# Kernel optimization log

Measured on AMD Instinct MI355X. Metric: run time of the kernel, lower is better.

## Reference

```python
import jax, jax.numpy as jnp
import numpy as np

B, S, D, H = 2, 2048, 512, 8
HD = D // H
DFF = 4 * D
EPS_LN = 1e-5
EPS_ATTN = 1e-8


def layernorm(x, w, b):
    mu = jnp.mean(x, axis=-1, keepdims=True)
    var = jnp.var(x, axis=-1, keepdims=True)
    return (x - mu) * jax.lax.rsqrt(var + EPS_LN) * w + b


def masked_attention(q_src, v_src, wq, bq, wk, bk, wv, bv, wo, bo, M):
    # q_src/v_src: (B,S,D); M: (B,S,S)
    Bs, Ss, _ = q_src.shape
    Q = (q_src @ wq + bq).reshape(Bs, Ss, H, HD)
    K = (q_src @ wk + bk).reshape(Bs, Ss, H, HD)
    V = (v_src @ wv + bv).reshape(Bs, Ss, H, HD)
    scale = HD ** -0.5
    scores = jnp.einsum('bqhd,bkhd->bhqk', Q, K) * scale
    Mh = M[:, None, :, :]                      # (B,1,S,S) broadcast over heads
    scores = scores * Mh
    A = jax.nn.softmax(scores, axis=-1)
    A = A * Mh                                 # re-mask post-softmax
    A = A / (jnp.sum(jnp.abs(A), axis=-1, keepdims=True) + EPS_ATTN)  # L1 renorm
    out = jnp.einsum('bhqk,bkhd->bqhd', A, V).reshape(Bs, Ss, D)
    return out @ wo + bo


def ffn(x, w1, b1, w2, b2):
    h = jax.nn.gelu(x @ w1 + b1, approximate=False)
    return x + (h @ w2 + b2)                   # FeedForward(num_layers=2) includes residual


def setup_inputs() -> dict:
    key = jax.random.key(0)
    ks = iter(jax.random.split(key, 64))
    nrm = lambda shape, s=0.02: jax.random.normal(next(ks), shape, jnp.float32) * s
    d = {
        'gene_emb': jax.random.normal(next(ks), (B, S, D), jnp.float32),
        'expr_emb': jax.random.normal(next(ks), (B, S, D), jnp.float32),
        'M': jax.random.uniform(next(ks), (B, S, S), jnp.float32),
    }
    # gene attention params (weights stored (in,out))
    for p in ['g_wq', 'g_wk', 'g_wv', 'g_wo']:
        d[p] = nrm((D, D))
    for p in ['g_bq', 'g_bk', 'g_bv', 'g_bo']:
        d[p] = jnp.zeros((D,), jnp.float32)
    # expr attention params (fused proj 2D->D)
    d['e_wf'] = nrm((2 * D, D)); d['e_bf'] = jnp.zeros((D,), jnp.float32)
    for p in ['e_wq', 'e_wk', 'e_wv', 'e_wo']:
        d[p] = nrm((D, D))
    for p in ['e_bq', 'e_bk', 'e_bv', 'e_bo']:
        d[p] = jnp.zeros((D,), jnp.float32)
    # layernorms
    for p in ['ln_g1_w', 'ln_g2_w', 'ln_e1_w', 'ln_e2_w']:
        d[p] = jnp.ones((D,), jnp.float32)
    for p in ['ln_g1_b', 'ln_g2_b', 'ln_e1_b', 'ln_e2_b']:
        d[p] = jnp.zeros((D,), jnp.float32)
    # FFNs
    d['fg_w1'] = nrm((D, DFF)); d['fg_b1'] = jnp.zeros((DFF,), jnp.float32)
    d['fg_w2'] = nrm((DFF, D)); d['fg_b2'] = jnp.zeros((D,), jnp.float32)
    d['fe_w1'] = nrm((D, DFF)); d['fe_b1'] = jnp.zeros((DFF,), jnp.float32)
    d['fe_w2'] = nrm((DFF, D)); d['fe_b2'] = jnp.zeros((D,), jnp.float32)
    return d


def reference(gene_emb, expr_emb, M,
              g_wq, g_bq, g_wk, g_bk, g_wv, g_bv, g_wo, g_bo,
              e_wf, e_bf, e_wq, e_bq, e_wk, e_bk, e_wv, e_bv, e_wo, e_bo,
              ln_g1_w, ln_g1_b, ln_g2_w, ln_g2_b,
              ln_e1_w, ln_e1_b, ln_e2_w, ln_e2_b,
              fg_w1, fg_b1, fg_w2, fg_b2,
              fe_w1, fe_b1, fe_w2, fe_b2):
    # ----- gene branch -----
    xg = layernorm(gene_emb, ln_g1_w, ln_g1_b)
    attn_g = masked_attention(xg, xg, g_wq, g_bq, g_wk, g_bk, g_wv, g_bv, g_wo, g_bo, M)
    x = gene_emb + attn_g
    x_ln = layernorm(x, ln_g2_w, ln_g2_b)
    out_gene = x + ffn(x_ln, fg_w1, fg_b1, fg_w2, fg_b2)
    # ----- expression branch -----
    y_n = layernorm(expr_emb, ln_e1_w, ln_e1_b)
    fused = jnp.concatenate([gene_emb, y_n], axis=-1) @ e_wf + e_bf
    attn_e = masked_attention(fused, y_n, e_wq, e_bq, e_wk, e_bk, e_wv, e_bv, e_wo, e_bo, M)
    y = expr_emb + attn_e
    y_ln = layernorm(y, ln_e2_w, ln_e2_b)
    out_expr = y + ffn(y_ln, fe_w1, fe_b1, fe_w2, fe_b2)
    return (out_gene, out_expr)
```

## Files before the change

kernel.cpp:

```cpp
#include <hip/hip_runtime.h>
#include <math.h>

#define S_LEN 2048
#define DMODEL 512
#define NROWS 4096
#define NHEAD 8
#define HDIM 64

typedef __attribute__((ext_vector_type(8))) __bf16 bf16x8;
typedef __attribute__((ext_vector_type(4))) float f32x4;

__device__ inline float bf2f(unsigned short h) {
    unsigned u = ((unsigned)h) << 16;
    return __builtin_bit_cast(float, u);
}
__device__ inline unsigned short f2bf(float f) {
    unsigned u = __builtin_bit_cast(unsigned, f);
    return (unsigned short)((u + 0x7fffu + ((u >> 16) & 1u)) >> 16);
}

__device__ inline void gl_lds16(const unsigned short* g, unsigned short* l) {
    __builtin_amdgcn_global_load_lds(
        (const __attribute__((address_space(1))) void*)g,
        (__attribute__((address_space(3))) void*)l, 16, 0, 0);
}

__global__ __launch_bounds__(256) void wcast_t(
    const float* __restrict__ W, unsigned short* __restrict__ Wt, int K, int Mo)
{
    __shared__ float t[32][33];
    const int bx = blockIdx.x * 32;
    const int by = blockIdx.y * 32;
    const int tx = threadIdx.x & 31, ty = threadIdx.x >> 5;
    #pragma unroll
    for (int r = 0; r < 4; ++r)
        t[ty + 8 * r][tx] = W[(size_t)(by + ty + 8 * r) * Mo + bx + tx];
    __syncthreads();
    #pragma unroll
    for (int r = 0; r < 4; ++r)
        Wt[(size_t)(bx + ty + 8 * r) * K + by + tx] = f2bf(t[tx][ty + 8 * r]);
}

__global__ __launch_bounds__(256) void wcast_sq8(
    const float* w0, const float* w1, const float* w2, const float* w3,
    const float* w4, const float* w5, const float* w6, const float* w7,
    unsigned short* __restrict__ dst)
{
    const float* srcs[8] = {w0, w1, w2, w3, w4, w5, w6, w7};
    const float* __restrict__ W = srcs[blockIdx.z];
    unsigned short* __restrict__ Wt = dst + (size_t)blockIdx.z * 512 * 512;
    __shared__ float t[32][33];
    const int bx = blockIdx.x * 32, by = blockIdx.y * 32;
    const int tx = threadIdx.x & 31, ty = threadIdx.x >> 5;
    #pragma unroll
    for (int r = 0; r < 4; ++r)
        t[ty + 8 * r][tx] = W[(size_t)(by + ty + 8 * r) * 512 + bx + tx];
    __syncthreads();
    #pragma unroll
    for (int r = 0; r < 4; ++r)
        Wt[(size_t)(bx + ty + 8 * r) * 512 + by + tx] = f2bf(t[tx][ty + 8 * r]);
}

__global__ __launch_bounds__(256) void wcast_t2(
    const float* wA, const float* wB, unsigned short* __restrict__ dst,
    int K, int Mo)
{
    const float* __restrict__ W = blockIdx.z ? wB : wA;
    unsigned short* __restrict__ Wt = dst + (size_t)blockIdx.z * K * Mo;
    __shared__ float t[32][33];
    const int bx = blockIdx.x * 32, by = blockIdx.y * 32;
    const int tx = threadIdx.x & 31, ty = threadIdx.x >> 5;
    #pragma unroll
    for (int r = 0; r < 4; ++r)
        t[ty + 8 * r][tx] = W[(size_t)(by + ty + 8 * r) * Mo + bx + tx];
    __syncthreads();
    #pragma unroll
    for (int r = 0; r < 4; ++r)
        Wt[(size_t)(bx + ty + 8 * r) * K + by + tx] = f2bf(t[tx][ty + 8 * r]);
}

__global__ __launch_bounds__(256) void pack_bias(
    const float* __restrict__ b1, const float* __restrict__ b2,
    const float* __restrict__ b3, float* __restrict__ dst, int n)
{
    int t = blockIdx.x * 256 + threadIdx.x;
    if (t >= n) return;
    float v = (t < 512) ? b1[t] : (t < 1024) ? b2[t - 512] : b3[t - 1024];
    dst[t] = v;
}

__global__ __launch_bounds__(256) void cast_strided(
    const float* __restrict__ in, unsigned short* __restrict__ out, int ostride)
{
    const int row = blockIdx.x, t = threadIdx.x;
    out[(size_t)row * ostride + t]       = f2bf(in[(size_t)row * DMODEL + t]);
    out[(size_t)row * ostride + t + 256] = f2bf(in[(size_t)row * DMODEL + t + 256]);
}

__global__ __launch_bounds__(256) void ln_kernel(
    const float* __restrict__ x, const float* __restrict__ w,
    const float* __restrict__ b, unsigned short* __restrict__ y, int ostride)
{
    __shared__ float red[8];
    const int row = blockIdx.x;
    const float* xr = x + (size_t)row * DMODEL;
    const int t = threadIdx.x;
    float v0 = xr[t];
    float v1 = xr[t + 256];
    float s  = v0 + v1;
    float sq = v0 * v0 + v1 * v1;
    #pragma unroll
    for (int o = 32; o > 0; o >>= 1) {
        s  += __shfl_down(s, o);
        sq += __shfl_down(sq, o);
    }
    int wid = t >> 6, lane = t & 63;
    if (lane == 0) { red[wid] = s; red[4 + wid] = sq; }
    __syncthreads();
    float mean = (red[0] + red[1] + red[2] + red[3]) * (1.0f / 512.0f);
    float msq  = (red[4] + red[5] + red[6] + red[7]) * (1.0f / 512.0f);
    float var  = msq - mean * mean;
    float rs   = rsqrtf(var + 1e-5f);
    y[(size_t)row * ostride + t]       = f2bf((v0 - mean) * rs * w[t] + b[t]);
    y[(size_t)row * ostride + t + 256] = f2bf((v1 - mean) * rs * w[t + 256] + b[t + 256]);
}

__global__ __launch_bounds__(256) void vtrans(
    const unsigned short* __restrict__ V, int ldv, unsigned short* __restrict__ Vt)
{
    __shared__ unsigned short t[64][72];
    const int s0 = blockIdx.x * 64, h = blockIdx.y, b = blockIdx.z;
    const int tid = threadIdx.x;
    {
        const int r = tid >> 2, c = (tid & 3) * 16;
        const unsigned short* src = V + (size_t)(b * S_LEN + s0 + r) * ldv + h * 64 + c;
        *(int4*)&t[r][c]     = *(const int4*)(src);
        *(int4*)&t[r][c + 8] = *(const int4*)(src + 8);
    }
    __syncthreads();
    {
        const int d = tid >> 2, s = (tid & 3) * 16;
        unsigned short* dst = Vt + ((size_t)((b * 8 + h) * 64 + d)) * S_LEN + s0 + s;
        unsigned short tmp[16];
        #pragma unroll
        for (int e = 0; e < 16; ++e) tmp[e] = t[s + e][d];
        *(int4*)dst       = *(int4*)&tmp[0];
        *(int4*)(dst + 8) = *(int4*)&tmp[8];
    }
}

__global__ __launch_bounds__(256) void gemm_mfma(
    const unsigned short* __restrict__ A, int lda,
    const unsigned short* __restrict__ Bt,
    const float* __restrict__ bias,
    const float* __restrict__ R1,
    const unsigned short* __restrict__ R2,
    float* __restrict__ Cf, unsigned short* __restrict__ Cb,
    int K, int Mo, int dogelu)
{
    __shared__ __align__(16) unsigned short As[128 * 32];
    __shared__ __align__(16) unsigned short Bs[128 * 32];
    const int tid = threadIdx.x;
    const int wave = tid >> 6, lane = tid & 63;
    const int wr = wave >> 1, wc = wave & 1;
    const int row0 = blockIdx.y * 128, col0 = blockIdx.x * 128;
    const int l15 = lane & 15, q = lane >> 4;

    f32x4 acc[4][4];
    const f32x4 zz = {0.f, 0.f, 0.f, 0.f};
    #pragma unroll
    for (int i = 0; i < 4; ++i)
        #pragma unroll
        for (int j = 0; j < 4; ++j) acc[i][j] = zz;

    for (int k0 = 0; k0 < K; k0 += 32) {
        #pragma unroll
        for (int r = 0; r < 2; ++r) {
            int idx = r * 256 + tid;
            int row = idx >> 2, kc = idx & 3;
            gl_lds16(&A[(size_t)(row0 + row) * lda + k0 + kc * 8],
                     &As[(size_t)(r * 256 + wave * 64) * 8]);
            gl_lds16(&Bt[(size_t)(col0 + row) * K + k0 + kc * 8],
                     &Bs[(size_t)(r * 256 + wave * 64) * 8]);
        }
        __syncthreads();
        bf16x8 af[4], bfr[4];
        #pragma unroll
        for (int fi = 0; fi < 4; ++fi)
            af[fi] = *(const bf16x8*)&As[(wr * 64 + fi * 16 + l15) * 32 + q * 8];
        #pragma unroll
        for (int fj = 0; fj < 4; ++fj)
            bfr[fj] = *(const bf16x8*)&Bs[(wc * 64 + fj * 16 + l15) * 32 + q * 8];
        #pragma unroll
        for (int fi = 0; fi < 4; ++fi)
            #pragma unroll
            for (int fj = 0; fj < 4; ++fj)
                acc[fi][fj] = __builtin_amdgcn_mfma_f32_16x16x32_bf16(
                    af[fi], bfr[fj], acc[fi][fj], 0, 0, 0);
        __syncthreads();
    }

    #pragma unroll
    for (int fi = 0; fi < 4; ++fi) {
        #pragma unroll
        for (int reg = 0; reg < 4; ++reg) {
            int row = row0 + wr * 64 + fi * 16 + q * 4 + reg;
            #pragma unroll
            for (int fj = 0; fj < 4; ++fj) {
                int col = col0 + wc * 64 + fj * 16 + l15;
                float v = acc[fi][fj][reg] + bias[col];
                if (dogelu) v = 0.5f * v * (1.0f + erff(v * 0.70710678118654752f));
                size_t off = (size_t)row * Mo + col;
                if (R1) v += R1[off];
                if (R2) v += bf2f(R2[off]);
                if (Cb) Cb[off] = f2bf(v);
                else    Cf[off] = v;
            }
        }
    }
}

__global__ __launch_bounds__(256) void gemm_mfma64(
    const unsigned short* __restrict__ A, int lda,
    const unsigned short* __restrict__ Bt,
    const float* __restrict__ bias,
    const float* __restrict__ R1,
    const unsigned short* __restrict__ R2,
    float* __restrict__ Cf, unsigned short* __restrict__ Cb,
    int K, int Mo, int dogelu)
{
    __shared__ __align__(16) unsigned short As[64 * 64];
    __shared__ __align__(16) unsigned short Bs[64 * 64];
    const int tid = threadIdx.x;
    const int wave = tid >> 6, lane = tid & 63;
    const int row0 = blockIdx.y * 64, col0 = blockIdx.x * 64;
    const int l15 = lane & 15, q = lane >> 4;

    f32x4 acc[4];
    const f32x4 zz = {0.f, 0.f, 0.f, 0.f};
    #pragma unroll
    for (int j = 0; j < 4; ++j) acc[j] = zz;

    for (int k0 = 0; k0 < K; k0 += 64) {
        #pragma unroll
        for (int r = 0; r < 2; ++r) {
            int idx = r * 256 + tid;
            int row = idx >> 3, kc = idx & 7;
            gl_lds16(&A[(size_t)(row0 + row) * lda + k0 + kc * 8],
                     &As[(size_t)(r * 256 + wave * 64) * 8]);
            gl_lds16(&Bt[(size_t)(col0 + row) * K + k0 + kc * 8],
                     &Bs[(size_t)(r * 256 + wave * 64) * 8]);
        }
        __syncthreads();
        #pragma unroll
        for (int ks = 0; ks < 2; ++ks) {
            bf16x8 af = *(const bf16x8*)&As[(wave * 16 + l15) * 64 + ks * 32 + q * 8];
            bf16x8 bfr[4];
            #pragma unroll
            for (int fj = 0; fj < 4; ++fj)
                bfr[fj] = *(const bf16x8*)&Bs[(fj * 16 + l15) * 64 + ks * 32 + q * 8];
            #pragma unroll
            for (int fj = 0; fj < 4; ++fj)
                acc[fj] = __builtin_amdgcn_mfma_f32_16x16x32_bf16(af, bfr[fj], acc[fj], 0, 0, 0);
        }
        __syncthreads();
    }

    #pragma unroll
    for (int reg = 0; reg < 4; ++reg) {
        int row = row0 + wave * 16 + q * 4 + reg;
        #pragma unroll
        for (int fj = 0; fj < 4; ++fj) {
            int col = col0 + fj * 16 + l15;
            float v = acc[fj][reg] + bias[col];
            if (dogelu) v = 0.5f * v * (1.0f + erff(v * 0.70710678118654752f));
            size_t off = (size_t)row * Mo + col;
            if (R1) v += R1[off];
            if (R2) v += bf2f(R2[off]);
            if (Cb) Cb[off] = f2bf(v);
            else    Cf[off] = v;
        }
    }
}

__global__ __launch_bounds__(256, 4) void attn_mfma_split(
    const unsigned short* __restrict__ Q, int ldq,
    const unsigned short* __restrict__ Kp, int ldk,
    const unsigned short* __restrict__ Vt,
    const float* __restrict__ M,
    unsigned short* __restrict__ Opart,
    float* __restrict__ stats)
{
    __shared__ __align__(16) unsigned short Ks[64 * 72];
    __shared__ __align__(16) unsigned short Vs[64 * 72];
    __shared__ __align__(16) float Ms[4][16 * 68];

    const int bh = blockIdx.y, b = bh >> 3, h = bh & 7;
    const int q0 = blockIdx.x * 64;
    const int p = blockIdx.z;
    const int tid = threadIdx.x, wave = tid >> 6, lane = tid & 63;
    const int l15 = lane & 15, quad = lane >> 4;
    const int iRow = q0 + wave * 16 + l15;
    const int kBeg = p * (S_LEN / 2), kEnd = kBeg + (S_LEN / 2);

    unsigned short* Ps = (unsigned short*)&Ms[wave][0];

    bf16x8 qf[2];
    {
        const unsigned short* qp = Q + (size_t)(b * S_LEN + iRow) * ldq + h * HDIM + quad * 8;
        #pragma unroll
        for (int ks = 0; ks < 2; ++ks) {
            union { bf16x8 v; unsigned short u[8]; } tq;
            tq.v = *(const bf16x8*)(qp + ks * 32);
            #pragma unroll
            for (int e = 0; e < 8; ++e) tq.u[e] = f2bf(bf2f(tq.u[e]) * 0.125f);
            qf[ks] = tq.v;
        }
    }

    float rm = -INFINITY, rZ = 0.f, rZm = 0.f;
    f32x4 oacc[4];
    const f32x4 zz = {0.f, 0.f, 0.f, 0.f};
    #pragma unroll
    for (int dt = 0; dt < 4; ++dt) oacc[dt] = zz;

    const int srow = tid >> 3;
    const int scol = (tid & 7) * 8;
    const unsigned short* kg = Kp + ((size_t)b * S_LEN) * ldk + h * HDIM + scol;
    const unsigned short* vg = Vt + ((size_t)bh * 64 + srow) * S_LEN + scol;
    const float* mg = M + (size_t)b * S_LEN * S_LEN + (size_t)(q0 + wave * 16) * S_LEN;

    for (int k0 = kBeg; k0 < kEnd; k0 += 64) {
        __syncthreads();
        int4 kv0 = *(const int4*)(kg + (size_t)(k0 + srow) * ldk);
        int4 kv1 = *(const int4*)(kg + (size_t)(k0 + srow + 32) * ldk);
        int4 vv0 = *(const int4*)(vg + k0);
        int4 vv1 = *(const int4*)(vg + 32 * S_LEN + k0);
        float4 mv[4];
        #pragma unroll
        for (int c = 0; c < 4; ++c)
            mv[c] = *(const float4*)(mg + (size_t)(c * 4 + quad) * S_LEN + k0 + l15 * 4);
        *(int4*)&Ks[srow * 72 + scol]        = kv0;
        *(int4*)&Ks[(srow + 32) * 72 + scol] = kv1;
        *(int4*)&Vs[srow * 72 + scol]        = vv0;
        *(int4*)&Vs[(srow + 32) * 72 + scol] = vv1;
        #pragma unroll
        for (int c = 0; c < 4; ++c)
            *(float4*)&Ms[wave][(c * 4 + quad) * 68 + l15 * 4] = mv[c];
        __syncthreads();

        float4 m4[4];
        #pragma unroll
        for (int jt = 0; jt < 4; ++jt)
            m4[jt] = *(const float4*)&Ms[wave][l15 * 68 + jt * 16 + quad * 4];

        f32x4 sacc[4];
        #pragma unroll
        for (int jt = 0; jt < 4; ++jt) sacc[jt] = zz;
        #pragma unroll
        for (int jt = 0; jt < 4; ++jt) {
            bf16x8 kf0 = *(const bf16x8*)&Ks[(jt * 16 + l15) * 72 + quad * 8];
            bf16x8 kf1 = *(const bf16x8*)&Ks[(jt * 16 + l15) * 72 + 32 + quad * 8];
            sacc[jt] = __builtin_amdgcn_mfma_f32_16x16x32_bf16(kf0, qf[0], sacc[jt], 0, 0, 0);
            sacc[jt] = __builtin_amdgcn_mfma_f32_16x16x32_bf16(kf1, qf[1], sacc[jt], 0, 0, 0);
        }

        float mx = -INFINITY;
        #pragma unroll
        for (int jt = 0; jt < 4; ++jt) {
            float mm[4] = {m4[jt].x, m4[jt].y, m4[jt].z, m4[jt].w};
            #pragma unroll
            for (int r = 0; r < 4; ++r) {
                sacc[jt][r] = sacc[jt][r] * mm[r];
                mx = fmaxf(mx, sacc[jt][r]);
            }
        }
        mx = fmaxf(mx, __shfl_xor(mx, 16));
        mx = fmaxf(mx, __shfl_xor(mx, 32));
        float mn = fmaxf(rm, mx);
        float al = __expf(rm - mn);
        rm = mn; rZ *= al; rZm *= al;
        #pragma unroll
        for (int dt = 0; dt < 4; ++dt)
            #pragma unroll
            for (int r = 0; r < 4; ++r) oacc[dt][r] *= al;

        float z = 0.f, zm = 0.f;
        #pragma unroll
        for (int jt = 0; jt < 4; ++jt) {
            float mm[4] = {m4[jt].x, m4[jt].y, m4[jt].z, m4[jt].w};
            float pv[4];
            #pragma unroll
            for (int r = 0; r < 4; ++r) {
                float e = __expf(sacc[jt][r] - mn);
                float pm = e * mm[r];
                z += e; zm += pm; pv[r] = pm;
            }
            unsigned lo = (unsigned)f2bf(pv[0]) | ((unsigned)f2bf(pv[1]) << 16);
            unsigned hi = (unsigned)f2bf(pv[2]) | ((unsigned)f2bf(pv[3]) << 16);
            uint2 pk; pk.x = lo; pk.y = hi;
            *(uint2*)&Ps[l15 * 72 + jt * 16 + quad * 4] = pk;
        }
        z  += __shfl_xor(z, 16);  z  += __shfl_xor(z, 32);
        zm += __shfl_xor(zm, 16); zm += __shfl_xor(zm, 32);
        rZ += z; rZm += zm;

        bf16x8 pf0 = *(const bf16x8*)&Ps[l15 * 72 + quad * 8];
        bf16x8 pf1 = *(const bf16x8*)&Ps[l15 * 72 + 32 + quad * 8];
        #pragma unroll
        for (int dt = 0; dt < 4; ++dt) {
            bf16x8 vf0 = *(const bf16x8*)&Vs[(dt * 16 + l15) * 72 + quad * 8];
            bf16x8 vf1 = *(const bf16x8*)&Vs[(dt * 16 + l15) * 72 + 32 + quad * 8];
            oacc[dt] = __builtin_amdgcn_mfma_f32_16x16x32_bf16(vf0, pf0, oacc[dt], 0, 0, 0);
            oacc[dt] = __builtin_amdgcn_mfma_f32_16x16x32_bf16(vf1, pf1, oacc[dt], 0, 0, 0);
        }
    }

    unsigned short* op = Opart + (((size_t)(p * 16 + bh) * S_LEN + iRow) * 64);
    #pragma unroll
    for (int dt = 0; dt < 4; ++dt) {
        ushort4 o4;
        o4.x = f2bf(oacc[dt][0]); o4.y = f2bf(oacc[dt][1]);
        o4.z = f2bf(oacc[dt][2]); o4.w = f2bf(oacc[dt][3]);
        *(ushort4*)(op + dt * 16 + quad * 4) = o4;
    }
    if (quad == 0) {
        float4 st; st.x = rm; st.y = rZ; st.z = rZm; st.w = 0.f;
        *(float4*)&stats[(((size_t)p * 16 + bh) * S_LEN + iRow) * 4] = st;
    }
}

__global__ __launch_bounds__(256) void attn_combine(
    const unsigned short* __restrict__ Opart, const float* __restrict__ stats,
    unsigned short* __restrict__ O)
{
    const int bh = blockIdx.y, b = bh >> 3, h = bh & 7;
    const int q0 = blockIdx.x * 64;
    const int tid = threadIdx.x;
    const int i = tid >> 2, dq = (tid & 3) * 16;
    const int qg = q0 + i;

    float4 s0 = *(const float4*)&stats[(((size_t)0 * 16 + bh) * S_LEN + qg) * 4];
    float4 s1 = *(const float4*)&stats[(((size_t)1 * 16 + bh) * S_LEN + qg) * 4];
    float ms = fmaxf(s0.x, s1.x);
    float w0 = __expf(s0.x - ms), w1 = __expf(s1.x - ms);
    float Z  = w0 * s0.y + w1 * s1.y;
    float Zm = w0 * s0.z + w1 * s1.z;
    float inv = 1.0f / (Zm + 1e-8f * Z);
    w0 *= inv; w1 *= inv;

    const unsigned short* p0 = Opart + (((size_t)0 * 16 + bh) * S_LEN + qg) * 64 + dq;
    const unsigned short* p1 = Opart + (((size_t)1 * 16 + bh) * S_LEN + qg) * 64 + dq;
    union { int4 v; unsigned short u[8]; } a0, a1, r;
    unsigned short* dst = O + (size_t)(b * S_LEN + qg) * DMODEL + h * HDIM + dq;
    #pragma unroll
    for (int half = 0; half < 2; ++half) {
        a0.v = *(const int4*)(p0 + half * 8);
        a1.v = *(const int4*)(p1 + half * 8);
        #pragma unroll
        for (int e = 0; e < 8; ++e)
            r.u[e] = f2bf(w0 * bf2f(a0.u[e]) + w1 * bf2f(a1.u[e]));
        *(int4*)(dst + half * 8) = r.v;
    }
}

extern "C" void kernel_launch(void* const* d_in, const int* in_sizes, int n_in,
                              void* d_out, int out_size, void* d_ws, size_t ws_size,
                              hipStream_t stream)
{
    const float* gene_emb = (const float*)d_in[0];
    const float* expr_emb = (const float*)d_in[1];
    const float* M        = (const float*)d_in[2];
    const float* g_wq = (const float*)d_in[3];
    const float* g_wk = (const float*)d_in[4];
    const float* g_wv = (const float*)d_in[5];
    const float* g_wo = (const float*)d_in[6];
    const float* g_bq = (const float*)d_in[7];
    const float* g_bk = (const float*)d_in[8];
    const float* g_bv = (const float*)d_in[9];
    const float* g_bo = (const float*)d_in[10];
    const float* e_wf = (const float*)d_in[11];
    const float* e_bf = (const float*)d_in[12];
    const float* e_wq = (const float*)d_in[13];
    const float* e_wk = (const float*)d_in[14];
    const float* e_wv = (const float*)d_in[15];
    const float* e_wo = (const float*)d_in[16];
    const float* e_bq = (const float*)d_in[17];
    const float* e_bk = (const float*)d_in[18];
    const float* e_bv = (const float*)d_in[19];
    const float* e_bo = (const float*)d_in[20];
    const float* ln_g1_w = (const float*)d_in[21];
    const float* ln_g2_w = (const float*)d_in[22];
    const float* ln_e1_w = (const float*)d_in[23];
    const float* ln_e2_w = (const float*)d_in[24];
    const float* ln_g1_b = (const float*)d_in[25];
    const float* ln_g2_b = (const float*)d_in[26];
    const float* ln_e1_b = (const float*)d_in[27];
    const float* ln_e2_b = (const float*)d_in[28];
    const float* fg_w1 = (const float*)d_in[29];
    const float* fg_b1 = (const float*)d_in[30];
    const float* fg_w2 = (const float*)d_in[31];
    const float* fg_b2 = (const float*)d_in[32];
    const float* fe_w1 = (const float*)d_in[33];
    const float* fe_b1 = (const float*)d_in[34];
    const float* fe_w2 = (const float*)d_in[35];
    const float* fe_b2 = (const float*)d_in[36];

    float* out_gene = (float*)d_out;
    float* out_expr = out_gene + (size_t)NROWS * DMODEL;

    char* ws = (char*)d_ws;
    const size_t MB1 = 1024 * 1024;
    unsigned short* bufA16  = (unsigned short*)(ws + 0 * MB1);
    unsigned short* bufAt16 = (unsigned short*)(ws + 4 * MB1);
    unsigned short* bufQKV  = (unsigned short*)(ws + 8 * MB1);
    unsigned short* bufQKe  = (unsigned short*)(ws + 8 * MB1);
    unsigned short* bufV16  = (unsigned short*)(ws + 16 * MB1);
    unsigned short* bufVt   = (unsigned short*)(ws + 20 * MB1);
    unsigned short* bufCat  = (unsigned short*)(ws + 24 * MB1);
    unsigned short* bufOp   = (unsigned short*)(ws + 24 * MB1);
    float*          bufSt   = (float*)(ws + 32 * MB1);
    float*          bufX    = (float*)(ws + 33 * MB1);
    unsigned short* bufH16  = (unsigned short*)(ws + 8 * MB1);
    char* wp = ws + 41 * MB1;
    unsigned short* sq8    = (unsigned short*)wp;
    unsigned short* gwq_t  = sq8 + 0 * 512 * 512;
    unsigned short* gwk_t  = sq8 + 1 * 512 * 512;
    unsigned short* gwv_t  = sq8 + 2 * 512 * 512;
    unsigned short* gwo_t  = sq8 + 3 * 512 * 512;
    unsigned short* ewq_t  = sq8 + 4 * 512 * 512;
    unsigned short* ewk_t  = sq8 + 5 * 512 * 512;
    unsigned short* ewv_t  = sq8 + 6 * 512 * 512;
    unsigned short* ewo_t  = sq8 + 7 * 512 * 512;
    unsigned short* ewf_t  = sq8 + 8 * 512 * 512;
    unsigned short* ffn1   = ewf_t + 1024 * 512;
    unsigned short* fgw1_t = ffn1;
    unsigned short* few1_t = ffn1 + 512 * 2048;
    unsigned short* ffn2   = few1_t + 512 * 2048;
    unsigned short* fgw2_t = ffn2;
    unsigned short* few2_t = ffn2 + 2048 * 512;
    float* biasg = (float*)(few2_t + 2048 * 512);
    float* biase = biasg + 1536;

    dim3 blk(256);
    dim3 ln_grid(NROWS);
    dim3 g512s(8, 64);
    dim3 g1024(8, 32);
    dim3 g1536(12, 32);
    dim3 g2048(16, 32);
    dim3 attn_grid(S_LEN / 64, 16, 2);
    dim3 comb_grid(S_LEN / 64, 16);
    dim3 vt_grid(S_LEN / 64, NHEAD, 2);

    wcast_sq8<<<dim3(16, 16, 8), blk, 0, stream>>>(
        g_wq, g_wk, g_wv, g_wo, e_wq, e_wk, e_wv, e_wo, sq8);
    wcast_t<<<dim3(16, 32), blk, 0, stream>>>(e_wf, ewf_t, 1024, 512);
    wcast_t2<<<dim3(64, 16, 2), blk, 0, stream>>>(fg_w1, fe_w1, ffn1, 512, 2048);
    wcast_t2<<<dim3(16, 64, 2), blk, 0, stream>>>(fg_w2, fe_w2, ffn2, 2048, 512);
    pack_bias<<<dim3(6), blk, 0, stream>>>(g_bq, g_bk, g_bv, biasg, 1536);
    pack_bias<<<dim3(4), blk, 0, stream>>>(e_bq, e_bk, e_bk, biase, 1024);

    ln_kernel<<<ln_grid, blk, 0, stream>>>(gene_emb, ln_g1_w, ln_g1_b, bufA16, 512);
    gemm_mfma<<<g1536, blk, 0, stream>>>(bufA16, 512, gwq_t, biasg, nullptr, nullptr, nullptr, bufQKV, 512, 1536, 0);
    vtrans<<<vt_grid, blk, 0, stream>>>(bufQKV + 1024, 1536, bufVt);
    attn_mfma_split<<<attn_grid, blk, 0, stream>>>(bufQKV, 1536, bufQKV + 512, 1536, bufVt, M, bufOp, bufSt);
    attn_combine<<<comb_grid, blk, 0, stream>>>(bufOp, bufSt, bufAt16);
    gemm_mfma64<<<g512s, blk, 0, stream>>>(bufAt16, 512, gwo_t, g_bo, gene_emb, nullptr, bufX, nullptr, 512, 512, 0);
    ln_kernel<<<ln_grid, blk, 0, stream>>>(bufX, ln_g2_w, ln_g2_b, bufA16, 512);
    gemm_mfma<<<g2048, blk, 0, stream>>>(bufA16, 512, fgw1_t, fg_b1, nullptr, nullptr, nullptr, bufH16, 512, 2048, 1);
    gemm_mfma64<<<g512s, blk, 0, stream>>>(bufH16, 2048, fgw2_t, fg_b2, bufX, bufA16, out_gene, nullptr, 2048, 512, 0);

    cast_strided<<<ln_grid, blk, 0, stream>>>(gene_emb, bufCat, 1024);
    ln_kernel<<<ln_grid, blk, 0, stream>>>(expr_emb, ln_e1_w, ln_e1_b, bufCat + 512, 1024);
    gemm_mfma64<<<g512s, blk, 0, stream>>>(bufCat, 1024, ewf_t, e_bf, nullptr, nullptr, nullptr, bufA16, 1024, 512, 0);
    gemm_mfma<<<g1024, blk, 0, stream>>>(bufA16, 512, ewq_t, biase, nullptr, nullptr, nullptr, bufQKe, 512, 1024, 0);
    gemm_mfma64<<<g512s, blk, 0, stream>>>(bufCat + 512, 1024, ewv_t, e_bv, nullptr, nullptr, nullptr, bufV16, 512, 512, 0);
    vtrans<<<vt_grid, blk, 0, stream>>>(bufV16, 512, bufVt);
    attn_mfma_split<<<attn_grid, blk, 0, stream>>>(bufQKe, 1024, bufQKe + 512, 1024, bufVt, M, bufOp, bufSt);
    attn_combine<<<comb_grid, blk, 0, stream>>>(bufOp, bufSt, bufAt16);
    gemm_mfma64<<<g512s, blk, 0, stream>>>(bufAt16, 512, ewo_t, e_bo, expr_emb, nullptr, bufX, nullptr, 512, 512, 0);
    ln_kernel<<<ln_grid, blk, 0, stream>>>(bufX, ln_e2_w, ln_e2_b, bufA16, 512);
    gemm_mfma<<<g2048, blk, 0, stream>>>(bufA16, 512, few1_t, fe_b1, nullptr, nullptr, nullptr, bufH16, 512, 2048, 1);
    gemm_mfma64<<<g512s, blk, 0, stream>>>(bufH16, 2048, few2_t, fe_b2, bufX, bufA16, out_expr, nullptr, 2048, 512, 0);
}
```

Baseline: 545.5 us.

## Batch gene and expression branches into dual kernels and drop attention split-K combine

Restructures the launch schedule so the gene and expression branches share launches: a fused pre-LN/cast kernel, dual V-projection, out-projection and LN2 kernels, and one attention launch covering both branches over the full key range. The split-K attention with its separate combine pass is removed, and normalisation is folded into the attention epilogue. K/V/mask loads in attention are now register-prefetched one tile ahead. FFN weights are recast into a shared slot between branches to shrink the workspace. The cost is fewer attention blocks per branch with longer key loops, plus added serial weight casts mid-stream.

```diff
diff --git a/kernel.cpp b/kernel.cpp
--- a/kernel.cpp
+++ b/kernel.cpp
@@ -61,79 +61,91 @@
         Wt[(size_t)(bx + ty + 8 * r) * 512 + by + tx] = f2bf(t[tx][ty + 8 * r]);
 }
 
-__global__ __launch_bounds__(256) void wcast_t2(
-    const float* wA, const float* wB, unsigned short* __restrict__ dst,
-    int K, int Mo)
-{
-    const float* __restrict__ W = blockIdx.z ? wB : wA;
-    unsigned short* __restrict__ Wt = dst + (size_t)blockIdx.z * K * Mo;
-    __shared__ float t[32][33];
-    const int bx = blockIdx.x * 32, by = blockIdx.y * 32;
-    const int tx = threadIdx.x & 31, ty = threadIdx.x >> 5;
-    #pragma unroll
-    for (int r = 0; r < 4; ++r)
-        t[ty + 8 * r][tx] = W[(size_t)(by + ty + 8 * r) * Mo + bx + tx];
+__global__ __launch_bounds__(256) void pack_bias5(
+    const float* __restrict__ b0, const float* __restrict__ b1,
+    const float* __restrict__ b2, const float* __restrict__ b3,
+    const float* __restrict__ b4, float* __restrict__ dst)
+{
+    int t = blockIdx.x * 256 + threadIdx.x;
+    const float* srcs[5] = {b0, b1, b2, b3, b4};
+    dst[t] = srcs[t >> 9][t & 511];
+}
+
+__global__ __launch_bounds__(256) void elem_pre(
+    const float* __restrict__ gene, const float* __restrict__ expr,
+    const float* __restrict__ wg, const float* __restrict__ bg,
+    const float* __restrict__ we, const float* __restrict__ be,
+    unsigned short* __restrict__ lng,
+    unsigned short* __restrict__ cat)
+{
+    __shared__ float red[16];
+    const int row = blockIdx.x, t = threadIdx.x;
+    float g0 = gene[(size_t)row * 512 + t], g1 = gene[(size_t)row * 512 + t + 256];
+    float e0 = expr[(size_t)row * 512 + t], e1 = expr[(size_t)row * 512 + t + 256];
+    float sg = g0 + g1, qg = g0 * g0 + g1 * g1;
+    float se = e0 + e1, qe = e0 * e0 + e1 * e1;
+    #pragma unroll
+    for (int o = 32; o > 0; o >>= 1) {
+        sg += __shfl_down(sg, o); qg += __shfl_down(qg, o);
+        se += __shfl_down(se, o); qe += __shfl_down(qe, o);
+    }
+    int wid = t >> 6, lane = t & 63;
+    if (lane == 0) { red[wid] = sg; red[4 + wid] = qg; red[8 + wid] = se; red[12 + wid] = qe; }
     __syncthreads();
-    #pragma unroll
-    for (int r = 0; r < 4; ++r)
-        Wt[(size_t)(bx + ty + 8 * r) * K + by + tx] = f2bf(t[tx][ty + 8 * r]);
-}
-
-__global__ __launch_bounds__(256) void pack_bias(
-    const float* __restrict__ b1, const float* __restrict__ b2,
-    const float* __restrict__ b3, float* __restrict__ dst, int n)
-{
-    int t = blockIdx.x * 256 + threadIdx.x;
-    if (t >= n) return;
-    float v = (t < 512) ? b1[t] : (t < 1024) ? b2[t - 512] : b3[t - 1024];
-    dst[t] = v;
-}
-
-__global__ __launch_bounds__(256) void cast_strided(
-    const float* __restrict__ in, unsigned short* __restrict__ out, int ostride)
-{
+    float mg_ = (red[0] + red[1] + red[2] + red[3]) * (1.0f / 512.0f);
+    float qg_ = (red[4] + red[5] + red[6] + red[7]) * (1.0f / 512.0f);
+    float me_ = (red[8] + red[9] + red[10] + red[11]) * (1.0f / 512.0f);
+    float qe_ = (red[12] + red[13] + red[14] + red[15]) * (1.0f / 512.0f);
+    float rg = rsqrtf(qg_ - mg_ * mg_ + 1e-5f);
+    float re = rsqrtf(qe_ - me_ * me_ + 1e-5f);
+    lng[(size_t)row * 512 + t]        = f2bf((g0 - mg_) * rg * wg[t] + bg[t]);
+    lng[(size_t)row * 512 + t + 256]  = f2bf((g1 - mg_) * rg * wg[t + 256] + bg[t + 256]);
+    cat[(size_t)row * 1024 + t]       = f2bf(g0);
+    cat[(size_t)row * 1024 + t + 256] = f2bf(g1);
+    cat[(size_t)row * 1024 + 512 + t]       = f2bf((e0 - me_) * re * we[t] + be[t]);
+    cat[(size_t)row * 1024 + 512 + t + 256] = f2bf((e1 - me_) * re * we[t + 256] + be[t + 256]);
+}
+
+__global__ __launch_bounds__(256) void ln2_dual(
+    const float* __restrict__ X0, const float* __restrict__ X1,
+    const float* __restrict__ w0, const float* __restrict__ b0,
+    const float* __restrict__ w1, const float* __restrict__ b1,
+    unsigned short* __restrict__ y0, unsigned short* __restrict__ y1)
+{
+    __shared__ float red[8];
+    const int br = blockIdx.y;
+    const float* x = br ? X1 : X0;
+    const float* w = br ? w1 : w0;
+    const float* b = br ? b1 : b0;
+    unsigned short* y = br ? y1 : y0;
     const int row = blockIdx.x, t = threadIdx.x;
-    out[(size_t)row * ostride + t]       = f2bf(in[(size_t)row * DMODEL + t]);
-    out[(size_t)row * ostride + t + 256] = f2bf(in[(size_t)row * DMODEL + t + 256]);
-}
-
-__global__ __launch_bounds__(256) void ln_kernel(
-    const float* __restrict__ x, const float* __restrict__ w,
-    const float* __restrict__ b, unsigned short* __restrict__ y, int ostride)
-{
-    __shared__ float red[8];
-    const int row = blockIdx.x;
-    const float* xr = x + (size_t)row * DMODEL;
-    const int t = threadIdx.x;
-    float v0 = xr[t];
-    float v1 = xr[t + 256];
-    float s  = v0 + v1;
-    float sq = v0 * v0 + v1 * v1;
-    #pragma unroll
-    for (int o = 32; o > 0; o >>= 1) {
-        s  += __shfl_down(s, o);
-        sq += __shfl_down(sq, o);
-    }
+    float v0 = x[(size_t)row * 512 + t], v1 = x[(size_t)row * 512 + t + 256];
+    float s = v0 + v1, q = v0 * v0 + v1 * v1;
+    #pragma unroll
+    for (int o = 32; o > 0; o >>= 1) { s += __shfl_down(s, o); q += __shfl_down(q, o); }
     int wid = t >> 6, lane = t & 63;
-    if (lane == 0) { red[wid] = s; red[4 + wid] = sq; }
+    if (lane == 0) { red[wid] = s; red[4 + wid] = q; }
     __syncthreads();
     float mean = (red[0] + red[1] + red[2] + red[3]) * (1.0f / 512.0f);
     float msq  = (red[4] + red[5] + red[6] + red[7]) * (1.0f / 512.0f);
-    float var  = msq - mean * mean;
-    float rs   = rsqrtf(var + 1e-5f);
-    y[(size_t)row * ostride + t]       = f2bf((v0 - mean) * rs * w[t] + b[t]);
-    y[(size_t)row * ostride + t + 256] = f2bf((v1 - mean) * rs * w[t + 256] + b[t + 256]);
-}
-
-__global__ __launch_bounds__(256) void vtrans(
-    const unsigned short* __restrict__ V, int ldv, unsigned short* __restrict__ Vt)
+    float rs = rsqrtf(msq - mean * mean + 1e-5f);
+    y[(size_t)row * 512 + t]       = f2bf((v0 - mean) * rs * w[t] + b[t]);
+    y[(size_t)row * 512 + t + 256] = f2bf((v1 - mean) * rs * w[t + 256] + b[t + 256]);
+}
+
+__global__ __launch_bounds__(256) void vtrans4(
+    const unsigned short* __restrict__ Vg, const unsigned short* __restrict__ Ve,
+    unsigned short* __restrict__ Vtg, unsigned short* __restrict__ Vte)
 {
     __shared__ unsigned short t[64][72];
-    const int s0 = blockIdx.x * 64, h = blockIdx.y, b = blockIdx.z;
+    const int z = blockIdx.z, branch = z >> 1, b = z & 1;
+    const unsigned short* V = branch ? Ve : Vg;
+    unsigned short* Vt = branch ? Vte : Vtg;
+    const int s0 = blockIdx.x * 64, h = blockIdx.y;
     const int tid = threadIdx.x;
     {
         const int r = tid >> 2, c = (tid & 3) * 16;
-        const unsigned short* src = V + (size_t)(b * S_LEN + s0 + r) * ldv + h * 64 + c;
+        const unsigned short* src = V + (size_t)(b * S_LEN + s0 + r) * 512 + h * 64 + c;
         *(int4*)&t[r][c]     = *(const int4*)(src);
         *(int4*)&t[r][c + 8] = *(const int4*)(src + 8);
     }
@@ -283,31 +295,103 @@
     }
 }
 
-__global__ __launch_bounds__(256, 4) void attn_mfma_split(
-    const unsigned short* __restrict__ Q, int ldq,
-    const unsigned short* __restrict__ Kp, int ldk,
-    const unsigned short* __restrict__ Vt,
+__global__ __launch_bounds__(256) void gemm64_dual(
+    const unsigned short* A0, const unsigned short* A1, int lda0, int lda1,
+    const unsigned short* W0, const unsigned short* W1,
+    const float* b0, const float* b1,
+    const float* R10, const float* R11,
+    float* Cf0, float* Cf1, unsigned short* Cb0, unsigned short* Cb1)
+{
+    __shared__ __align__(16) unsigned short As[64 * 64];
+    __shared__ __align__(16) unsigned short Bs[64 * 64];
+    const int j = blockIdx.z;
+    const unsigned short* __restrict__ A = j ? A1 : A0;
+    const int lda = j ? lda1 : lda0;
+    const unsigned short* __restrict__ Bt = j ? W1 : W0;
+    const float* __restrict__ bias = j ? b1 : b0;
+    const float* __restrict__ R1 = j ? R11 : R10;
+    float* __restrict__ Cf = j ? Cf1 : Cf0;
+    unsigned short* __restrict__ Cb = j ? Cb1 : Cb0;
+
+    const int tid = threadIdx.x;
+    const int wave = tid >> 6, lane = tid & 63;
+    const int row0 = blockIdx.y * 64, col0 = blockIdx.x * 64;
+    const int l15 = lane & 15, q = lane >> 4;
+
+    f32x4 acc[4];
+    const f32x4 zz = {0.f, 0.f, 0.f, 0.f};
+    #pragma unroll
+    for (int jj = 0; jj < 4; ++jj) acc[jj] = zz;
+
+    for (int k0 = 0; k0 < 512; k0 += 64) {
+        #pragma unroll
+        for (int r = 0; r < 2; ++r) {
+            int idx = r * 256 + tid;
+            int row = idx >> 3, kc = idx & 7;
+            gl_lds16(&A[(size_t)(row0 + row) * lda + k0 + kc * 8],
+                     &As[(size_t)(r * 256 + wave * 64) * 8]);
+            gl_lds16(&Bt[(size_t)(col0 + row) * 512 + k0 + kc * 8],
+                     &Bs[(size_t)(r * 256 + wave * 64) * 8]);
+        }
+        __syncthreads();
+        #pragma unroll
+        for (int ks = 0; ks < 2; ++ks) {
+            bf16x8 af = *(const bf16x8*)&As[(wave * 16 + l15) * 64 + ks * 32 + q * 8];
+            bf16x8 bfr[4];
+            #pragma unroll
+            for (int fj = 0; fj < 4; ++fj)
+                bfr[fj] = *(const bf16x8*)&Bs[(fj * 16 + l15) * 64 + ks * 32 + q * 8];
+            #pragma unroll
+            for (int fj = 0; fj < 4; ++fj)
+                acc[fj] = __builtin_amdgcn_mfma_f32_16x16x32_bf16(af, bfr[fj], acc[fj], 0, 0, 0);
+        }
+        __syncthreads();
+    }
+
+    #pragma unroll
+    for (int reg = 0; reg < 4; ++reg) {
+        int row = row0 + wave * 16 + q * 4 + reg;
+        #pragma unroll
+        for (int fj = 0; fj < 4; ++fj) {
+            int col = col0 + fj * 16 + l15;
+            float v = acc[fj][reg] + bias[col];
+            size_t off = (size_t)row * 512 + col;
+            if (R1) v += R1[off];
+            if (Cb) Cb[off] = f2bf(v);
+            else    Cf[off] = v;
+        }
+    }
+}
+
+__global__ __launch_bounds__(256, 4) void attn_fused(
+    const unsigned short* __restrict__ QKg,
+    const unsigned short* __restrict__ QKe,
+    const unsigned short* __restrict__ Vtg,
+    const unsigned short* __restrict__ Vte,
     const float* __restrict__ M,
-    unsigned short* __restrict__ Opart,
-    float* __restrict__ stats)
+    unsigned short* __restrict__ Og,
+    unsigned short* __restrict__ Oe)
 {
     __shared__ __align__(16) unsigned short Ks[64 * 72];
     __shared__ __align__(16) unsigned short Vs[64 * 72];
     __shared__ __align__(16) float Ms[4][16 * 68];
 
+    const int br = blockIdx.z;
+    const unsigned short* QK = br ? QKe : QKg;
+    const unsigned short* Vt = br ? Vte : Vtg;
+    unsigned short* O = br ? Oe : Og;
+
     const int bh = blockIdx.y, b = bh >> 3, h = bh & 7;
     const int q0 = blockIdx.x * 64;
-    const int p = blockIdx.z;
     const int tid = threadIdx.x, wave = tid >> 6, lane = tid & 63;
     const int l15 = lane & 15, quad = lane >> 4;
     const int iRow = q0 + wave * 16 + l15;
-    const int kBeg = p * (S_LEN / 2), kEnd = kBeg + (S_LEN / 2);
 
     unsigned short* Ps = (unsigned short*)&Ms[wave][0];
 
     bf16x8 qf[2];
     {
-        const unsigned short* qp = Q + (size_t)(b * S_LEN + iRow) * ldq + h * HDIM + quad * 8;
+        const unsigned short* qp = QK + (size_t)(b * S_LEN + iRow) * 1024 + h * HDIM + quad * 8;
         #pragma unroll
         for (int ks = 0; ks < 2; ++ks) {
             union { bf16x8 v; unsigned short u[8]; } tq;
@@ -326,27 +410,38 @@
 
     const int srow = tid >> 3;
     const int scol = (tid & 7) * 8;
-    const unsigned short* kg = Kp + ((size_t)b * S_LEN) * ldk + h * HDIM + scol;
+    const unsigned short* kg = QK + 512 + ((size_t)b * S_LEN) * 1024 + h * HDIM + scol;
     const unsigned short* vg = Vt + ((size_t)bh * 64 + srow) * S_LEN + scol;
     const float* mg = M + (size_t)b * S_LEN * S_LEN + (size_t)(q0 + wave * 16) * S_LEN;
 
-    for (int k0 = kBeg; k0 < kEnd; k0 += 64) {
-        __syncthreads();
-        int4 kv0 = *(const int4*)(kg + (size_t)(k0 + srow) * ldk);
-        int4 kv1 = *(const int4*)(kg + (size_t)(k0 + srow + 32) * ldk);
-        int4 vv0 = *(const int4*)(vg + k0);
-        int4 vv1 = *(const int4*)(vg + 32 * S_LEN + k0);
-        float4 mv[4];
+    int4 pK0 = *(const int4*)(kg + (size_t)(srow) * 1024);
+    int4 pK1 = *(const int4*)(kg + (size_t)(srow + 32) * 1024);
+    int4 pV0 = *(const int4*)(vg);
+    int4 pV1 = *(const int4*)(vg + 32 * S_LEN);
+    float4 pM[4];
+    #pragma unroll
+    for (int c = 0; c < 4; ++c)
+        pM[c] = *(const float4*)(mg + (size_t)(c * 4 + quad) * S_LEN + l15 * 4);
+
+    for (int k0 = 0; k0 < S_LEN; k0 += 64) {
+        __syncthreads();
+        *(int4*)&Ks[srow * 72 + scol]        = pK0;
+        *(int4*)&Ks[(srow + 32) * 72 + scol] = pK1;
+        *(int4*)&Vs[srow * 72 + scol]        = pV0;
+        *(int4*)&Vs[(srow + 32) * 72 + scol] = pV1;
         #pragma unroll
         for (int c = 0; c < 4; ++c)
-            mv[c] = *(const float4*)(mg + (size_t)(c * 4 + quad) * S_LEN + k0 + l15 * 4);
-        *(int4*)&Ks[srow * 72 + scol]        = kv0;
-        *(int4*)&Ks[(srow + 32) * 72 + scol] = kv1;
-        *(int4*)&Vs[srow * 72 + scol]        = vv0;
-        *(int4*)&Vs[(srow + 32) * 72 + scol] = vv1;
-        #pragma unroll
-        for (int c = 0; c < 4; ++c)
-            *(float4*)&Ms[wave][(c * 4 + quad) * 68 + l15 * 4] = mv[c];
+            *(float4*)&Ms[wave][(c * 4 + quad) * 68 + l15 * 4] = pM[c];
+        int kn = k0 + 64;
+        if (kn < S_LEN) {
+            pK0 = *(const int4*)(kg + (size_t)(kn + srow) * 1024);
+            pK1 = *(const int4*)(kg + (size_t)(kn + srow + 32) * 1024);
+            pV0 = *(const int4*)(vg + kn);
+            pV1 = *(const int4*)(vg + 32 * S_LEN + kn);
+            #pragma unroll
+            for (int c = 0; c < 4; ++c)
+                pM[c] = *(const float4*)(mg + (size_t)(c * 4 + quad) * S_LEN + kn + l15 * 4);
+        }
         __syncthreads();
 
         float4 m4[4];
@@ -416,51 +511,13 @@
         }
     }
 
-    unsigned short* op = Opart + (((size_t)(p * 16 + bh) * S_LEN + iRow) * 64);
+    float inv = 1.0f / (rZm + 1e-8f * rZ);
     #pragma unroll
     for (int dt = 0; dt < 4; ++dt) {
         ushort4 o4;
-        o4.x = f2bf(oacc[dt][0]); o4.y = f2bf(oacc[dt][1]);
-        o4.z = f2bf(oacc[dt][2]); o4.w = f2bf(oacc[dt][3]);
-        *(ushort4*)(op + dt * 16 + quad * 4) = o4;
-    }
-    if (quad == 0) {
-        float4 st; st.x = rm; st.y = rZ; st.z = rZm; st.w = 0.f;
-        *(float4*)&stats[(((size_t)p * 16 + bh) * S_LEN + iRow) * 4] = st;
-    }
-}
-
-__global__ __launch_bounds__(256) void attn_combine(
-    const unsigned short* __restrict__ Opart, const float* __restrict__ stats,
-    unsigned short* __restrict__ O)
-{
-    const int bh = blockIdx.y, b = bh >> 3, h = bh & 7;
-    const int q0 = blockIdx.x * 64;
-    const int tid = threadIdx.x;
-    const int i = tid >> 2, dq = (tid & 3) * 16;
-    const int qg = q0 + i;
-
-    float4 s0 = *(const float4*)&stats[(((size_t)0 * 16 + bh) * S_LEN + qg) * 4];
-    float4 s1 = *(const float4*)&stats[(((size_t)1 * 16 + bh) * S_LEN + qg) * 4];
-    float ms = fmaxf(s0.x, s1.x);
-    float w0 = __expf(s0.x - ms), w1 = __expf(s1.x - ms);
-    float Z  = w0 * s0.y + w1 * s1.y;
-    float Zm = w0 * s0.z + w1 * s1.z;
-    float inv = 1.0f / (Zm + 1e-8f * Z);
-    w0 *= inv; w1 *= inv;
-
-    const unsigned short* p0 = Opart + (((size_t)0 * 16 + bh) * S_LEN + qg) * 64 + dq;
-    const unsigned short* p1 = Opart + (((size_t)1 * 16 + bh) * S_LEN + qg) * 64 + dq;
-    union { int4 v; unsigned short u[8]; } a0, a1, r;
-    unsigned short* dst = O + (size_t)(b * S_LEN + qg) * DMODEL + h * HDIM + dq;
-    #pragma unroll
-    for (int half = 0; half < 2; ++half) {
-        a0.v = *(const int4*)(p0 + half * 8);
-        a1.v = *(const int4*)(p1 + half * 8);
-        #pragma unroll
-        for (int e = 0; e < 8; ++e)
-            r.u[e] = f2bf(w0 * bf2f(a0.u[e]) + w1 * bf2f(a1.u[e]));
-        *(int4*)(dst + half * 8) = r.v;
+        o4.x = f2bf(oacc[dt][0] * inv); o4.y = f2bf(oacc[dt][1] * inv);
+        o4.z = f2bf(oacc[dt][2] * inv); o4.w = f2bf(oacc[dt][3] * inv);
+        *(ushort4*)(O + (size_t)(b * S_LEN + iRow) * DMODEL + h * HDIM + dt * 16 + quad * 4) = o4;
     }
 }
 
@@ -511,75 +568,75 @@
 
     char* ws = (char*)d_ws;
     const size_t MB1 = 1024 * 1024;
-    unsigned short* bufA16  = (unsigned short*)(ws + 0 * MB1);
-    unsigned short* bufAt16 = (unsigned short*)(ws + 4 * MB1);
-    unsigned short* bufQKV  = (unsigned short*)(ws + 8 * MB1);
-    unsigned short* bufQKe  = (unsigned short*)(ws + 8 * MB1);
-    unsigned short* bufV16  = (unsigned short*)(ws + 16 * MB1);
-    unsigned short* bufVt   = (unsigned short*)(ws + 20 * MB1);
-    unsigned short* bufCat  = (unsigned short*)(ws + 24 * MB1);
-    unsigned short* bufOp   = (unsigned short*)(ws + 24 * MB1);
-    float*          bufSt   = (float*)(ws + 32 * MB1);
-    float*          bufX    = (float*)(ws + 33 * MB1);
-    unsigned short* bufH16  = (unsigned short*)(ws + 8 * MB1);
-    char* wp = ws + 41 * MB1;
-    unsigned short* sq8    = (unsigned short*)wp;
-    unsigned short* gwq_t  = sq8 + 0 * 512 * 512;
-    unsigned short* gwk_t  = sq8 + 1 * 512 * 512;
+    unsigned short* sq8    = (unsigned short*)(ws);
     unsigned short* gwv_t  = sq8 + 2 * 512 * 512;
     unsigned short* gwo_t  = sq8 + 3 * 512 * 512;
-    unsigned short* ewq_t  = sq8 + 4 * 512 * 512;
-    unsigned short* ewk_t  = sq8 + 5 * 512 * 512;
+    unsigned short* ewqk_t = sq8 + 4 * 512 * 512;
     unsigned short* ewv_t  = sq8 + 6 * 512 * 512;
     unsigned short* ewo_t  = sq8 + 7 * 512 * 512;
-    unsigned short* ewf_t  = sq8 + 8 * 512 * 512;
-    unsigned short* ffn1   = ewf_t + 1024 * 512;
-    unsigned short* fgw1_t = ffn1;
-    unsigned short* few1_t = ffn1 + 512 * 2048;
-    unsigned short* ffn2   = few1_t + 512 * 2048;
-    unsigned short* fgw2_t = ffn2;
-    unsigned short* few2_t = ffn2 + 2048 * 512;
-    float* biasg = (float*)(few2_t + 2048 * 512);
-    float* biase = biasg + 1536;
+    unsigned short* ewf_t  = (unsigned short*)(ws + 4 * MB1);
+    unsigned short* w1slot = (unsigned short*)(ws + 5 * MB1);
+    unsigned short* w2slot = (unsigned short*)(ws + 7 * MB1);
+    float* biasAll = (float*)(ws + 9 * MB1);
+
+    unsigned short* bufLNg = (unsigned short*)(ws + 10 * MB1);
+    unsigned short* bufFe  = (unsigned short*)(ws + 10 * MB1);
+    unsigned short* bufAtg = (unsigned short*)(ws + 10 * MB1);
+    unsigned short* bufCat = (unsigned short*)(ws + 14 * MB1);
+    float*          bufXg  = (float*)(ws + 14 * MB1);
+    unsigned short* bufQKg = (unsigned short*)(ws + 22 * MB1);
+    float*          bufXe  = (float*)(ws + 22 * MB1);
+    unsigned short* bufQKe = (unsigned short*)(ws + 30 * MB1);
+    unsigned short* bufA16g = (unsigned short*)(ws + 30 * MB1);
+    unsigned short* bufA16e = (unsigned short*)(ws + 34 * MB1);
+    unsigned short* bufVg  = (unsigned short*)(ws + 38 * MB1);
+    unsigned short* bufAte = (unsigned short*)(ws + 38 * MB1);
+    unsigned short* bufVe  = (unsigned short*)(ws + 42 * MB1);
+    unsigned short* bufVtg = (unsigned short*)(ws + 46 * MB1);
+    unsigned short* bufVte = (unsigned short*)(ws + 50 * MB1);
+    unsigned short* bufHid = (unsigned short*)(ws + 38 * MB1);
 
     dim3 blk(256);
-    dim3 ln_grid(NROWS);
-    dim3 g512s(8, 64);
-    dim3 g1024(8, 32);
-    dim3 g1536(12, 32);
-    dim3 g2048(16, 32);
+    dim3 gQK(8, 32);
+    dim3 gFFN1(16, 32);
+    dim3 g64(8, 64);
+    dim3 g64d(8, 64, 2);
     dim3 attn_grid(S_LEN / 64, 16, 2);
-    dim3 comb_grid(S_LEN / 64, 16);
-    dim3 vt_grid(S_LEN / 64, NHEAD, 2);
+    dim3 vt_grid(S_LEN / 64, NHEAD, 4);
 
     wcast_sq8<<<dim3(16, 16, 8), blk, 0, stream>>>(
         g_wq, g_wk, g_wv, g_wo, e_wq, e_wk, e_wv, e_wo, sq8);
     wcast_t<<<dim3(16, 32), blk, 0, stream>>>(e_wf, ewf_t, 1024, 512);
-    wcast_t2<<<dim3(64, 16, 2), blk, 0, stream>>>(fg_w1, fe_w1, ffn1, 512, 2048);
-    wcast_t2<<<dim3(16, 64, 2), blk, 0, stream>>>(fg_w2, fe_w2, ffn2, 2048, 512);
-    pack_bias<<<dim3(6), blk, 0, stream>>>(g_bq, g_bk, g_bv, biasg, 1536);
-    pack_bias<<<dim3(4), blk, 0, stream>>>(e_bq, e_bk, e_bk, biase, 1024);
-
-    ln_kernel<<<ln_grid, blk, 0, stream>>>(gene_emb, ln_g1_w, ln_g1_b, bufA16, 512);
-    gemm_mfma<<<g1536, blk, 0, stream>>>(bufA16, 512, gwq_t, biasg, nullptr, nullptr, nullptr, bufQKV, 512, 1536, 0);
-    vtrans<<<vt_grid, blk, 0, stream>>>(bufQKV + 1024, 1536, bufVt);
-    attn_mfma_split<<<attn_grid, blk, 0, stream>>>(bufQKV, 1536, bufQKV + 512, 1536, bufVt, M, bufOp, bufSt);
-    attn_combine<<<comb_grid, blk, 0, stream>>>(bufOp, bufSt, bufAt16);
-    gemm_mfma64<<<g512s, blk, 0, stream>>>(bufAt16, 512, gwo_t, g_bo, gene_emb, nullptr, bufX, nullptr, 512, 512, 0);
-    ln_kernel<<<ln_grid, blk, 0, stream>>>(bufX, ln_g2_w, ln_g2_b, bufA16, 512);
-    gemm_mfma<<<g2048, blk, 0, stream>>>(bufA16, 512, fgw1_t, fg_b1, nullptr, nullptr, nullptr, bufH16, 512, 2048, 1);
-    gemm_mfma64<<<g512s, blk, 0, stream>>>(bufH16, 2048, fgw2_t, fg_b2, bufX, bufA16, out_gene, nullptr, 2048, 512, 0);
-
-    cast_strided<<<ln_grid, blk, 0, stream>>>(gene_emb, bufCat, 1024);
-    ln_kernel<<<ln_grid, blk, 0, stream>>>(expr_emb, ln_e1_w, ln_e1_b, bufCat + 512, 1024);
-    gemm_mfma64<<<g512s, blk, 0, stream>>>(bufCat, 1024, ewf_t, e_bf, nullptr, nullptr, nullptr, bufA16, 1024, 512, 0);
-    gemm_mfma<<<g1024, blk, 0, stream>>>(bufA16, 512, ewq_t, biase, nullptr, nullptr, nullptr, bufQKe, 512, 1024, 0);
-    gemm_mfma64<<<g512s, blk, 0, stream>>>(bufCat + 512, 1024, ewv_t, e_bv, nullptr, nullptr, nullptr, bufV16, 512, 512, 0);
-    vtrans<<<vt_grid, blk, 0, stream>>>(bufV16, 512, bufVt);
-    attn_mfma_split<<<attn_grid, blk, 0, stream>>>(bufQKe, 1024, bufQKe + 512, 1024, bufVt, M, bufOp, bufSt);
-    attn_combine<<<comb_grid, blk, 0, stream>>>(bufOp, bufSt, bufAt16);
-    gemm_mfma64<<<g512s, blk, 0, stream>>>(bufAt16, 512, ewo_t, e_bo, expr_emb, nullptr, bufX, nullptr, 512, 512, 0);
-    ln_kernel<<<ln_grid, blk, 0, stream>>>(bufX, ln_e2_w, ln_e2_b, bufA16, 512);
-    gemm_mfma<<<g2048, blk, 0, stream>>>(bufA16, 512, few1_t, fe_b1, nullptr, nullptr, nullptr, bufH16, 512, 2048, 1);
-    gemm_mfma64<<<g512s, blk, 0, stream>>>(bufH16, 2048, few2_t, fe_b2, bufX, bufA16, out_expr, nullptr, 2048, 512, 0);
-}
+    wcast_t<<<dim3(64, 16), blk, 0, stream>>>(fg_w1, w1slot, 512, 2048);
+    wcast_t<<<dim3(16, 64), blk, 0, stream>>>(fg_w2, w2slot, 2048, 512);
+    pack_bias5<<<dim3(10), blk, 0, stream>>>(g_bq, g_bk, g_bv, e_bq, e_bk, biasAll);
+
+    elem_pre<<<dim3(NROWS), blk, 0, stream>>>(
+        gene_emb, expr_emb, ln_g1_w, ln_g1_b, ln_e1_w, ln_e1_b, bufLNg, bufCat);
+
+    gemm64_dual<<<g64d, blk, 0, stream>>>(
+        bufLNg, bufCat + 512, 512, 1024, gwv_t, ewv_t, biasAll + 1024, e_bv,
+        nullptr, nullptr, nullptr, nullptr, bufVg, bufVe);
+    vtrans4<<<vt_grid, blk, 0, stream>>>(bufVg, bufVe, bufVtg, bufVte);
+
+    gemm_mfma<<<gQK, blk, 0, stream>>>(bufLNg, 512, sq8, biasAll, nullptr, nullptr, nullptr, bufQKg, 512, 1024, 0);
+    gemm_mfma64<<<g64, blk, 0, stream>>>(bufCat, 1024, ewf_t, e_bf, nullptr, nullptr, nullptr, bufFe, 1024, 512, 0);
+    gemm_mfma<<<gQK, blk, 0, stream>>>(bufFe, 512, ewqk_t, biasAll + 1536, nullptr, nullptr, nullptr, bufQKe, 512, 1024, 0);
+
+    attn_fused<<<attn_grid, blk, 0, stream>>>(bufQKg, bufQKe, bufVtg, bufVte, M, bufAtg, bufAte);
+
+    gemm64_dual<<<g64d, blk, 0, stream>>>(
+        bufAtg, bufAte, 512, 512, gwo_t, ewo_t, g_bo, e_bo,
+        gene_emb, expr_emb, bufXg, bufXe, nullptr, nullptr);
+
+    ln2_dual<<<dim3(NROWS, 2), blk, 0, stream>>>(
+        bufXg, bufXe, ln_g2_w, ln_g2_b, ln_e2_w, ln_e2_b, bufA16g, bufA16e);
+
+    gemm_mfma<<<gFFN1, blk, 0, stream>>>(bufA16g, 512, w1slot, fg_b1, nullptr, nullptr, nullptr, bufHid, 512, 2048, 1);
+    gemm_mfma64<<<g64, blk, 0, stream>>>(bufHid, 2048, w2slot, fg_b2, bufXg, bufA16g, out_gene, nullptr, 2048, 512, 0);
+
+    wcast_t<<<dim3(64, 16), blk, 0, stream>>>(fe_w1, w1slot, 512, 2048);
+    wcast_t<<<dim3(16, 64), blk, 0, stream>>>(fe_w2, w2slot, 2048, 512);
+    gemm_mfma<<<gFFN1, blk, 0, stream>>>(bufA16e, 512, w1slot, fe_b1, nullptr, nullptr, nullptr, bufHid, 512, 2048, 1);
+    gemm_mfma64<<<g64, blk, 0, stream>>>(bufHid, 2048, w2slot, fe_b2, bufXe, bufA16e, out_expr, nullptr, 2048, 512, 0);
+}
```

After: 617.9 us. 13.3% more time.
